# Kernel tuning notes

Measured on AMD Instinct MI355X. Metric: run time of the kernel, lower is better.

The kernel has to match this reference:

```python
import jax, jax.numpy as jnp
import numpy as np

N_LAYERS, D_MODEL, H, D_K, D_V, D_FF, VOCAB = 6, 512, 8, 64, 64, 2048, 32000
B, S = 4, 512
NEG_INF = -jnp.inf


def positional_encoding(seq_len, d_model):
    # Faithful to the (buggy-vs-paper) source: angle = pos / 10000**(2*i/d_model),
    # sin for even i, cos for odd i (i is the raw channel index).
    pos = jnp.arange(seq_len, dtype=jnp.float32)[:, None]
    i = jnp.arange(d_model, dtype=jnp.float32)[None, :]
    angle = pos / jnp.power(10000.0, 2.0 * i / d_model)
    return jnp.where((jnp.arange(d_model) % 2 == 0)[None, :], jnp.sin(angle), jnp.cos(angle))


def layer_norm(x, g, b, eps=1e-5):
    mu = jnp.mean(x, -1, keepdims=True)
    var = jnp.mean((x - mu) ** 2, -1, keepdims=True)
    return (x - mu) * jax.lax.rsqrt(var + eps) * g + b


def mha(q_in, k_in, v_in, wq, wk, wv, wo, q_mask, k_mask, causal):
    # wq/wk: (H, D, D_K), wv: (H, D, D_V), wo: (H*D_V, D)
    q = jnp.einsum('bsd,hdk->bhsk', q_in, wq)
    k = jnp.einsum('btd,hdk->bhtk', k_in, wk)
    v = jnp.einsum('btd,hdk->bhtk', v_in, wv)
    scores = jnp.einsum('bhsk,bhtk->bhst', q, k) / jnp.sqrt(jnp.float32(D_K))
    allowed = q_mask[:, None, :, None] & k_mask[:, None, None, :]  # (B,1,S,T)
    if causal:
        sl, tl = q_in.shape[1], k_in.shape[1]
        allowed = allowed & (jnp.arange(tl)[None, :] <= jnp.arange(sl)[:, None])[None, None]
    scores = jnp.where(allowed, scores, NEG_INF)
    attn = jax.nn.softmax(scores, axis=-1)
    out = jnp.einsum('bhst,bhtk->bshk', attn, v)  # (B,S,H,D_V)
    out = out.reshape(out.shape[0], out.shape[1], H * D_V)
    return out @ wo


def ffn(x, w1, b1, w2, b2):
    return jax.nn.relu(x @ w1 + b1) @ w2 + b2


def setup_inputs() -> dict:
    key = jax.random.key(0)
    ks = iter(jax.random.split(key, 40))
    f = lambda shape, scale: (jax.random.normal(next(ks), shape, dtype=jnp.float32) * scale)
    inp = {
        'src_tokens': jax.random.randint(next(ks), (B, S), 0, VOCAB),
        'tgt_tokens': jax.random.randint(next(ks), (B, S), 0, VOCAB),
        'src_mask': jnp.ones((B, S), dtype=bool),
        'tgt_mask': jnp.ones((B, S), dtype=bool),
        'embed': f((VOCAB, D_MODEL), 0.02),
        'enc_wqkv': f((N_LAYERS, 3, H, D_MODEL, D_K), 0.04),
        'enc_wo': f((N_LAYERS, H * D_V, D_MODEL), 0.04),
        'enc_ff_w1': f((N_LAYERS, D_MODEL, D_FF), 0.02),
        'enc_ff_b1': jnp.zeros((N_LAYERS, D_FF), jnp.float32),
        'enc_ff_w2': f((N_LAYERS, D_FF, D_MODEL), 0.02),
        'enc_ff_b2': jnp.zeros((N_LAYERS, D_MODEL), jnp.float32),
        'enc_ln_g': jnp.ones((N_LAYERS, 2, D_MODEL), jnp.float32),
        'enc_ln_b': jnp.zeros((N_LAYERS, 2, D_MODEL), jnp.float32),
        'dec_wqkv1': f((N_LAYERS, 3, H, D_MODEL, D_K), 0.04),
        'dec_wo1': f((N_LAYERS, H * D_V, D_MODEL), 0.04),
        'dec_wqkv2': f((N_LAYERS, 3, H, D_MODEL, D_K), 0.04),
        'dec_wo2': f((N_LAYERS, H * D_V, D_MODEL), 0.04),
        'dec_ff_w1': f((N_LAYERS, D_MODEL, D_FF), 0.02),
        'dec_ff_b1': jnp.zeros((N_LAYERS, D_FF), jnp.float32),
        'dec_ff_w2': f((N_LAYERS, D_FF, D_MODEL), 0.02),
        'dec_ff_b2': jnp.zeros((N_LAYERS, D_MODEL), jnp.float32),
        'dec_ln_g': jnp.ones((N_LAYERS, 3, D_MODEL), jnp.float32),
        'dec_ln_b': jnp.zeros((N_LAYERS, 3, D_MODEL), jnp.float32),
        'out_w': f((D_MODEL, VOCAB), 0.02),
        'out_b': jnp.zeros((VOCAB,), jnp.float32),
    }
    return inp


def reference(src_tokens, tgt_tokens, src_mask, tgt_mask, embed,
              enc_wqkv, enc_wo, enc_ff_w1, enc_ff_b1, enc_ff_w2, enc_ff_b2, enc_ln_g, enc_ln_b,
              dec_wqkv1, dec_wo1, dec_wqkv2, dec_wo2, dec_ff_w1, dec_ff_b1, dec_ff_w2, dec_ff_b2,
              dec_ln_g, dec_ln_b, out_w, out_b):
    pe = positional_encoding(src_tokens.shape[1], D_MODEL)
    x = embed[src_tokens] + pe[None]
    for i in range(N_LAYERS):
        a = mha(x, x, x, enc_wqkv[i, 0], enc_wqkv[i, 1], enc_wqkv[i, 2], enc_wo[i], src_mask, src_mask, False)
        x = layer_norm(x + a, enc_ln_g[i, 0], enc_ln_b[i, 0])
        x = layer_norm(x + ffn(x, enc_ff_w1[i], enc_ff_b1[i], enc_ff_w2[i], enc_ff_b2[i]), enc_ln_g[i, 1], enc_ln_b[i, 1])
    pe_t = positional_encoding(tgt_tokens.shape[1], D_MODEL)
    y = embed[tgt_tokens] + pe_t[None]
    for i in range(N_LAYERS):
        a = mha(y, y, y, dec_wqkv1[i, 0], dec_wqkv1[i, 1], dec_wqkv1[i, 2], dec_wo1[i], tgt_mask, tgt_mask, True)
        y = layer_norm(y + a, dec_ln_g[i, 0], dec_ln_b[i, 0])
        a = mha(y, x, x, dec_wqkv2[i, 0], dec_wqkv2[i, 1], dec_wqkv2[i, 2], dec_wo2[i], tgt_mask, src_mask, False)
        y = layer_norm(y + a, dec_ln_g[i, 1], dec_ln_b[i, 1])
        y = layer_norm(y + ffn(y, dec_ff_w1[i], dec_ff_b1[i], dec_ff_w2[i], dec_ff_b2[i]), dec_ln_g[i, 2], dec_ln_b[i, 2])
    return y @ out_w + out_b
```

## Files before the change

### kernel.cpp

```cpp
#include <hip/hip_runtime.h>
#include <math.h>


typedef unsigned short u16;
typedef __attribute__((ext_vector_type(8))) short short8;
typedef __attribute__((ext_vector_type(4))) float f32x4;

__device__ __forceinline__ u16 f2bf(float f){
  unsigned u = __float_as_uint(f);
  return (u16)((u + 0x7fffu + ((u >> 16) & 1u)) >> 16);
}

#define GLDS16(gp, lp) __builtin_amdgcn_global_load_lds( \
    (const __attribute__((address_space(1))) unsigned int*)(const void*)(gp), \
    (__attribute__((address_space(3))) unsigned int*)(void*)(lp), 16, 0, 0)

__global__ __launch_bounds__(256) void embed_pe_kernel(
    const int* __restrict__ tok, const float* __restrict__ emb,
    float* __restrict__ out, u16* __restrict__ outh)
{
  int row = blockIdx.x;
  int s = row & 511;
  int t = tok[row];
  #pragma unroll
  for (int j = 0; j < 2; j++){
    int d = threadIdx.x + 256*j;
    float ang = (float)s * powf(10000.0f, -2.0f*(float)d/512.0f);
    float pe = (d & 1) ? cosf(ang) : sinf(ang);
    float v = emb[(size_t)t*512 + d] + pe;
    out[(size_t)row*512 + d] = v;
    outh[(size_t)row*512 + d] = f2bf(v);
  }
}

struct WDesc { const float* W; unsigned long long gs, ds; u16* dst; int K; int nx; int end; };
struct WPack { WDesc d[6]; };

__global__ __launch_bounds__(256) void wcast_multi(WPack P, int nseg){
  int blk = blockIdx.x, s = 0;
  while (s < nseg-1 && blk >= P.d[s].end) s++;
  WDesc D = P.d[s];
  int base = s ? P.d[s-1].end : 0;
  int lb = blk - base;
  int g = lb % D.nx, kt = lb / D.nx;
  __shared__ u16 T[64][65];
  int tid = threadIdx.x;
  const float* Wb = D.W + (size_t)g*D.gs + (size_t)kt*64*D.ds;
  #pragma unroll
  for (int i = 0; i < 16; i++){
    int li = tid + 256*i;
    int kk = li >> 6, c = li & 63;
    T[kk][c] = f2bf(Wb[(size_t)kk*D.ds + c]);
  }
  __syncthreads();
  #pragma unroll
  for (int i = 0; i < 16; i++){
    int lo = tid + 256*i;
    int c = lo >> 6, kk = lo & 63;
    D.dst[(size_t)(g*64 + c)*D.K + kt*64 + kk] = T[kk][c];
  }
}

__global__ __launch_bounds__(256) void flash_attn_kernel(
    const u16* __restrict__ qkv, const u16* __restrict__ vT,
    u16* __restrict__ ctx, int causal)
{
  __shared__ __align__(16) u16 lQ[64*64];
  __shared__ __align__(16) u16 lK[2][64*64];
  __shared__ __align__(16) u16 lV[2][64*64];
  __shared__ __align__(16) u16 lP[4][16*64];
  int tid = threadIdx.x, lane = tid & 63, w = tid >> 6;
  int r16 = lane & 15, l4 = lane >> 4;
  int bh = blockIdx.x >> 3, qb = blockIdx.x & 7;
  int b = bh >> 3, h = bh & 7;
  const u16* qbase = qkv + (size_t)b*512*1536 + h*64;

  #pragma unroll
  for (int i = 0; i < 2; i++){
    int idx = i*256 + tid;
    int r = idx >> 3, c = idx & 7;
    GLDS16(qbase + (size_t)(qb*64 + r)*1536 + ((c ^ (r & 7))*8),
           lQ + (i*256 + w*64)*8);
  }
  auto stageKV = [&](int buf, int tt){
    #pragma unroll
    for (int i = 0; i < 2; i++){
      int idx = i*256 + tid;
      int r = idx >> 3, c = idx & 7;
      GLDS16(qbase + 512 + (size_t)(tt*64 + r)*1536 + ((c ^ (r & 7))*8),
             lK[buf] + (i*256 + w*64)*8);
      GLDS16(vT + ((size_t)bh*64 + r)*512 + tt*64 + ((c ^ (r & 7))*8),
             lV[buf] + (i*256 + w*64)*8);
    }
  };
  stageKV(0, 0);
  __syncthreads();
  short8 qa[2];
  #pragma unroll
  for (int kt = 0; kt < 2; kt++){
    int q = w*16 + r16;
    qa[kt] = *(const short8*)&lQ[q*64 + (((kt*4 + l4) ^ (q & 7))*8)];
  }

  f32x4 o[4];
  float mrow[4], lrow[4];
  #pragma unroll
  for (int j = 0; j < 4; j++){ o[j] = (f32x4){0.f,0.f,0.f,0.f}; mrow[j] = -3e38f; lrow[j] = 0.f; }

  int ntl = causal ? (qb + 1) : 8;
  int buf = 0;
  for (int tt = 0; tt < ntl; tt++){
    if (tt + 1 < ntl) stageKV(buf ^ 1, tt + 1);
    f32x4 s[4];
    #pragma unroll
    for (int ct = 0; ct < 4; ct++) s[ct] = (f32x4){0.f,0.f,0.f,0.f};
    __builtin_amdgcn_s_setprio(1);
    #pragma unroll
    for (int kt = 0; kt < 2; kt++){
      #pragma unroll
      for (int ct = 0; ct < 4; ct++){
        int trow = ct*16 + r16;
        short8 kb = *(const short8*)&lK[buf][trow*64 + (((kt*4 + l4) ^ (trow & 7))*8)];
        s[ct] = __builtin_amdgcn_mfma_f32_16x16x32_bf16(qa[kt], kb, s[ct], 0, 0, 0);
      }
    }
    __builtin_amdgcn_s_setprio(0);
    float p[4][4];
    #pragma unroll
    for (int ct = 0; ct < 4; ct++)
      #pragma unroll
      for (int r = 0; r < 4; r++){
        float v = s[ct][r] * 0.125f;
        if (causal && tt == qb && (ct*16 + r16) > (w*16 + l4*4 + r)) v = -1e30f;
        p[ct][r] = v;
      }
    #pragma unroll
    for (int r = 0; r < 4; r++){
      float pm = fmaxf(fmaxf(p[0][r], p[1][r]), fmaxf(p[2][r], p[3][r]));
      #pragma unroll
      for (int off = 1; off < 16; off <<= 1) pm = fmaxf(pm, __shfl_xor(pm, off));
      float mn = fmaxf(mrow[r], pm);
      float scl = __expf(mrow[r] - mn);
      mrow[r] = mn;
      float rs = 0.f;
      #pragma unroll
      for (int ct = 0; ct < 4; ct++){ p[ct][r] = __expf(p[ct][r] - mn); rs += p[ct][r]; }
      #pragma unroll
      for (int off = 1; off < 16; off <<= 1) rs += __shfl_xor(rs, off);
      lrow[r] = lrow[r]*scl + rs;
      #pragma unroll
      for (int jf = 0; jf < 4; jf++) o[jf][r] *= scl;
    }
    u16* myP = &lP[w][0];
    #pragma unroll
    for (int ct = 0; ct < 4; ct++)
      #pragma unroll
      for (int r = 0; r < 4; r++){
        int q = l4*4 + r, t = ct*16 + r16;
        myP[q*64 + (((t >> 3) ^ (q & 7))*8) + (t & 7)] = f2bf(p[ct][r]);
      }
    __builtin_amdgcn_s_setprio(1);
    #pragma unroll
    for (int kt = 0; kt < 2; kt++){
      short8 pa = *(const short8*)&myP[r16*64 + (((kt*4 + l4) ^ (r16 & 7))*8)];
      #pragma unroll
      for (int jf = 0; jf < 4; jf++){
        int dr = jf*16 + r16;
        short8 vv = *(const short8*)&lV[buf][dr*64 + (((kt*4 + l4) ^ (dr & 7))*8)];
        o[jf] = __builtin_amdgcn_mfma_f32_16x16x32_bf16(pa, vv, o[jf], 0, 0, 0);
      }
    }
    __builtin_amdgcn_s_setprio(0);
    __syncthreads();
    buf ^= 1;
  }
  #pragma unroll
  for (int r = 0; r < 4; r++){
    float inv = 1.0f / lrow[r];
    int q = qb*64 + w*16 + l4*4 + r;
    u16* dst = ctx + (size_t)(b*512 + q)*512 + h*64;
    #pragma unroll
    for (int jf = 0; jf < 4; jf++)
      dst[jf*16 + r16] = f2bf(o[jf][r] * inv);
  }
}

__global__ __launch_bounds__(256) void ln_kernel(
    float* __restrict__ x, const float* __restrict__ res,
    const float* __restrict__ g, const float* __restrict__ bt,
    u16* __restrict__ xh)
{
  int tid = threadIdx.x, lane = tid & 63, wv = tid >> 6;
  int row = blockIdx.x*4 + wv;
  size_t base = (size_t)row*512;
  float v[8]; float sum = 0.f;
  #pragma unroll
  for (int j = 0; j < 8; j++){
    int d = lane + 64*j;
    v[j] = x[base + d] + res[base + d];
    sum += v[j];
  }
  #pragma unroll
  for (int o = 32; o; o >>= 1) sum += __shfl_xor(sum, o);
  float mu = sum * (1.0f/512.0f);
  float vs = 0.f;
  #pragma unroll
  for (int j = 0; j < 8; j++){ float dd = v[j] - mu; vs += dd*dd; }
  #pragma unroll
  for (int o = 32; o; o >>= 1) vs += __shfl_xor(vs, o);
  float rstd = rsqrtf(vs*(1.0f/512.0f) + 1e-5f);
  #pragma unroll
  for (int j = 0; j < 8; j++){
    int d = lane + 64*j;
    float ov = (v[j] - mu)*rstd*g[d] + bt[d];
    x[base + d] = ov;
    xh[base + d] = f2bf(ov);
  }
}

template<int BM, int BN, int WM, int WN, int VOUT>
__global__ __launch_bounds__(WM*WN*64) void mfma_gemm(
    const u16* __restrict__ A, int lda,
    const u16* __restrict__ B, int ldb,
    void* __restrict__ C, int ldc, int cbf,
    const float* __restrict__ bias, int relu, int K, u16* __restrict__ vt)
{
  constexpr int NT  = WM*WN*64;
  constexpr int SM  = BM/WM, SN = BN/WN;
  constexpr int FM  = SM/16, FN = SN/16;
  constexpr int RPS = NT/8;
  constexpr int AG  = BM/RPS, BG = BN/RPS;
  __shared__ __align__(16) u16 lA[2][BM*64];
  __shared__ __align__(16) u16 lB[2][BN*64];
  int tid = threadIdx.x, lane = tid & 63, w = tid >> 6;
  int wm = w / WN, wn = w % WN;
  int r16 = lane & 15, l4 = lane >> 4;
  int sr = (w << 3) + (lane >> 3);
  int sc = lane & 7;
  int scs = sc ^ (sr & 7);
  const u16* Ab = A + (size_t)blockIdx.y*BM*lda + (size_t)sr*lda + scs*8;
  const u16* Bb = B + (size_t)blockIdx.x*BN*ldb + (size_t)sr*ldb + scs*8;
  f32x4 acc[FM][FN];
  #pragma unroll
  for (int i = 0; i < FM; i++)
    #pragma unroll
    for (int j = 0; j < FN; j++)
      acc[i][j] = (f32x4){0.f, 0.f, 0.f, 0.f};

  auto stage = [&](int buf, int kt){
    #pragma unroll
    for (int s = 0; s < AG; s++)
      GLDS16(Ab + (size_t)(s*RPS)*lda + kt, &lA[buf][(s*RPS + (w << 3))*64]);
    #pragma unroll
    for (int s = 0; s < BG; s++)
      GLDS16(Bb + (size_t)(s*RPS)*ldb + kt, &lB[buf][(s*RPS + (w << 3))*64]);
  };
  stage(0, 0);
  int nk = K >> 6, cur = 0;
  for (int kt = 0; kt < nk; kt++){
    __syncthreads();
    if (kt + 1 < nk) stage(cur ^ 1, (kt + 1) << 6);
    #pragma unroll
    for (int ks = 0; ks < 2; ks++){
      short8 av[FM], bv[FN];
      #pragma unroll
      for (int i = 0; i < FM; i++){
        int row = wm*SM + i*16 + r16;
        av[i] = *(const short8*)&lA[cur][row*64 + (((ks*4 + l4) ^ (row & 7))*8)];
      }
      #pragma unroll
      for (int j = 0; j < FN; j++){
        int row = wn*SN + j*16 + r16;
        bv[j] = *(const short8*)&lB[cur][row*64 + (((ks*4 + l4) ^ (row & 7))*8)];
      }
      #pragma unroll
      for (int i = 0; i < FM; i++)
        #pragma unroll
        for (int j = 0; j < FN; j++)
          acc[i][j] = __builtin_amdgcn_mfma_f32_16x16x32_bf16(av[i], bv[j], acc[i][j], 0, 0, 0);
    }
    cur ^= 1;
  }

  if constexpr (VOUT){
    int nblk = blockIdx.x * BN;
    if (nblk >= 1024){
      constexpr int TP = BM + 4;
      u16* T = (u16*)&lA[0][0];
      __syncthreads();
      #pragma unroll
      for (int i = 0; i < FM; i++){
        int t0 = wm*SM + i*16 + l4*4;
        #pragma unroll
        for (int j = 0; j < FN; j++){
          int d = wn*SN + j*16 + r16;
          unsigned q01 = (unsigned)f2bf(acc[i][j][0]) | ((unsigned)f2bf(acc[i][j][1]) << 16);
          unsigned q23 = (unsigned)f2bf(acc[i][j][2]) | ((unsigned)f2bf(acc[i][j][3]) << 16);
          uint2 pk; pk.x = q01; pk.y = q23;
          *(uint2*)&T[d*TP + t0] = pk;
        }
      }
      __syncthreads();
      int h = (nblk - 1024) >> 6;
      int b = (blockIdx.y * BM) >> 9;
      int t0g = (blockIdx.y * BM) & 511;
      u16* dst = vt + (size_t)(b*8 + h)*64*512;
      constexpr int TQL = (BM == 128) ? 5 : 4;
      constexpr int NIT = (BM*64) / (NT*4);
      #pragma unroll
      for (int it = 0; it < NIT; it++){
        int idx = it*NT + tid;
        int d = idx >> TQL, tq = (idx & ((1 << TQL) - 1))*4;
        *(uint2*)&dst[(size_t)d*512 + t0g + tq] = *(const uint2*)&T[d*TP + tq];
      }
      return;
    }
  }

  int m0 = blockIdx.y*BM + wm*SM, n0 = blockIdx.x*BN + wn*SN;
  int r4 = l4*4;
  #pragma unroll
  for (int i = 0; i < FM; i++){
    #pragma unroll
    for (int j = 0; j < FN; j++){
      int col = n0 + j*16 + r16;
      float bi = bias ? bias[col] : 0.f;
      #pragma unroll
      for (int r = 0; r < 4; r++){
        int rowg = m0 + i*16 + r4 + r;
        float o = acc[i][j][r] + bi;
        if (relu) o = fmaxf(o, 0.f);
        if (cbf) ((u16*)C)[(size_t)rowg*ldc + col] = f2bf(o);
        else     ((float*)C)[(size_t)rowg*ldc + col] = o;
      }
    }
  }
}

__global__ __launch_bounds__(256) void xattn_qkv_gemm(
    const u16* __restrict__ Ay, const u16* __restrict__ Ax,
    const u16* __restrict__ Bt, u16* __restrict__ C, u16* __restrict__ vt)
{
  constexpr int BM=64, BN=64, WM=2, WN=2, NT=256;
  constexpr int SM=BM/WM, SN=BN/WN, FM=SM/16, FN=SN/16, RPS=NT/8;
  constexpr int AG=BM/RPS, BG=BN/RPS;
  __shared__ __align__(16) u16 lA[2][BM*64];
  __shared__ __align__(16) u16 lB[2][BN*64];
  int tid = threadIdx.x, lane = tid & 63, w = tid >> 6;
  int wm = w / WN, wn = w % WN;
  int r16 = lane & 15, l4 = lane >> 4;
  int sr = (w << 3) + (lane >> 3);
  int sc = lane & 7;
  int scs = sc ^ (sr & 7);
  int z = blockIdx.z;
  const u16* A = (z == 0) ? Ay : Ax;
  const u16* Ab = A + (size_t)blockIdx.y*BM*512 + (size_t)sr*512 + scs*8;
  const u16* Bb = Bt + (size_t)(z*512 + blockIdx.x*BN)*512 + (size_t)sr*512 + scs*8;
  f32x4 acc[FM][FN];
  #pragma unroll
  for (int i = 0; i < FM; i++)
    #pragma unroll
    for (int j = 0; j < FN; j++)
      acc[i][j] = (f32x4){0.f, 0.f, 0.f, 0.f};
  auto stage = [&](int buf, int kt){
    #pragma unroll
    for (int s = 0; s < AG; s++)
      GLDS16(Ab + (size_t)(s*RPS)*512 + kt, &lA[buf][(s*RPS + (w << 3))*64]);
    #pragma unroll
    for (int s = 0; s < BG; s++)
      GLDS16(Bb + (size_t)(s*RPS)*512 + kt, &lB[buf][(s*RPS + (w << 3))*64]);
  };
  stage(0, 0);
  int cur = 0;
  for (int kt = 0; kt < 8; kt++){
    __syncthreads();
    if (kt + 1 < 8) stage(cur ^ 1, (kt + 1) << 6);
    #pragma unroll
    for (int ks = 0; ks < 2; ks++){
      short8 av[FM], bv[FN];
      #pragma unroll
      for (int i = 0; i < FM; i++){
        int row = wm*SM + i*16 + r16;
        av[i] = *(const short8*)&lA[cur][row*64 + (((ks*4 + l4) ^ (row & 7))*8)];
      }
      #pragma unroll
      for (int j = 0; j < FN; j++){
        int row = wn*SN + j*16 + r16;
        bv[j] = *(const short8*)&lB[cur][row*64 + (((ks*4 + l4) ^ (row & 7))*8)];
      }
      #pragma unroll
      for (int i = 0; i < FM; i++)
        #pragma unroll
        for (int j = 0; j < FN; j++)
          acc[i][j] = __builtin_amdgcn_mfma_f32_16x16x32_bf16(av[i], bv[j], acc[i][j], 0, 0, 0);
    }
    cur ^= 1;
  }
  if (z == 2){
    constexpr int TP = BM + 4;
    u16* T = (u16*)&lA[0][0];
    __syncthreads();
    #pragma unroll
    for (int i = 0; i < FM; i++){
      int t0 = wm*SM + i*16 + l4*4;
      #pragma unroll
      for (int j = 0; j < FN; j++){
        int d = wn*SN + j*16 + r16;
        unsigned q01 = (unsigned)f2bf(acc[i][j][0]) | ((unsigned)f2bf(acc[i][j][1]) << 16);
        unsigned q23 = (unsigned)f2bf(acc[i][j][2]) | ((unsigned)f2bf(acc[i][j][3]) << 16);
        uint2 pk; pk.x = q01; pk.y = q23;
        *(uint2*)&T[d*TP + t0] = pk;
      }
    }
    __syncthreads();
    int h = blockIdx.x;
    int b = (blockIdx.y * BM) >> 9;
    int t0g = (blockIdx.y * BM) & 511;
    u16* dst = vt + (size_t)(b*8 + h)*64*512;
    #pragma unroll
    for (int it = 0; it < 1; it++){ }
    #pragma unroll
    for (int it = 0; it < (BM*64)/(NT*4); it++){
      int idx = it*NT + tid;
      int d = idx >> 4, tq = (idx & 15)*4;
      *(uint2*)&dst[(size_t)d*512 + t0g + tq] = *(const uint2*)&T[d*TP + tq];
    }
    return;
  }
  int m0 = blockIdx.y*BM + wm*SM, n0 = z*512 + blockIdx.x*BN + wn*SN;
  int r4 = l4*4;
  #pragma unroll
  for (int i = 0; i < FM; i++)
    #pragma unroll
    for (int j = 0; j < FN; j++)
      #pragma unroll
      for (int r = 0; r < 4; r++){
        int rowg = m0 + i*16 + r4 + r;
        C[(size_t)rowg*1536 + n0 + j*16 + r16] = f2bf(acc[i][j][r]);
      }
}

extern "C" void kernel_launch(void* const* d_in, const int* in_sizes, int n_in,
                              void* d_out, int out_size, void* d_ws, size_t ws_size,
                              hipStream_t stream)
{
  (void)in_sizes; (void)n_in; (void)out_size; (void)ws_size;
  const int*   src_tok   = (const int*)  d_in[0];
  const int*   tgt_tok   = (const int*)  d_in[1];
  const float* emb       = (const float*)d_in[4];
  const float* enc_wqkv  = (const float*)d_in[5];
  const float* enc_wo    = (const float*)d_in[6];
  const float* enc_ff_w1 = (const float*)d_in[7];
  const float* enc_ff_b1 = (const float*)d_in[8];
  const float* enc_ff_w2 = (const float*)d_in[9];
  const float* enc_ff_b2 = (const float*)d_in[10];
  const float* enc_ln_g  = (const float*)d_in[11];
  const float* enc_ln_b  = (const float*)d_in[12];
  const float* dec_wqkv1 = (const float*)d_in[13];
  const float* dec_wo1   = (const float*)d_in[14];
  const float* dec_wqkv2 = (const float*)d_in[15];
  const float* dec_wo2   = (const float*)d_in[16];
  const float* dec_ff_w1 = (const float*)d_in[17];
  const float* dec_ff_b1 = (const float*)d_in[18];
  const float* dec_ff_w2 = (const float*)d_in[19];
  const float* dec_ff_b2 = (const float*)d_in[20];
  const float* dec_ln_g  = (const float*)d_in[21];
  const float* dec_ln_b  = (const float*)d_in[22];
  const float* out_w     = (const float*)d_in[23];
  const float* out_b     = (const float*)d_in[24];
  float* outp = (float*)d_out;

  const size_t MB = 1024*1024;
  char* wsb = (char*)d_ws;
  float* xb     = (float*)(wsb + 0*MB);
  float* yb     = (float*)(wsb + 4*MB);
  u16*   xh     = (u16*)  (wsb + 8*MB);
  u16*   ctxb   = (u16*)  (wsb + 10*MB);
  u16*   yh     = (u16*)  (wsb + 12*MB);
  u16*   qkvb   = (u16*)  (wsb + 14*MB);
  u16*   vT     = (u16*)  (wsb + 20*MB);
  u16*   hid    = (u16*)  (wsb + 14*MB);
  u16*   sQKV   = (u16*)  (wsb + 22*MB);
  u16*   sWO    = (u16*)  (wsb + 23*MB + 512*1024);
  u16*   sFF1   = (u16*)  (wsb + 24*MB);
  u16*   sFF2   = (u16*)  (wsb + 26*MB);
  float* proj   = (float*)(wsb + 28*MB);
  u16*   wvbuf  = (u16*)  (wsb + 0*MB);

  auto g64 = [&](const u16* A,int lda,const u16* B,int ldb,void* C,int ldc,
                 int cbf,const float* bias,int relu,int M,int N,int K){
    mfma_gemm<64,64,2,2,0><<<dim3(N/64, M/64), 256, 0, stream>>>(
        A,lda,B,ldb,C,ldc,cbf,bias,relu,K,nullptr);
  };
  auto gqkv = [&](const u16* A,const u16* B,u16* C,u16* vt,int M){
    mfma_gemm<128,64,2,2,1><<<dim3(24, M/128), 256, 0, stream>>>(
        A,512,B,512,C,1536,1,nullptr,0,512,vt);
  };
  auto g12864 = [&](const u16* A,int lda,const u16* B,int ldb,void* C,int ldc,
                    int cbf,const float* bias,int relu,int M,int N,int K){
    mfma_gemm<128,64,2,2,0><<<dim3(N/64, M/128), 256, 0, stream>>>(
        A,lda,B,ldb,C,ldc,cbf,bias,relu,K,nullptr);
  };
  auto g128 = [&](const u16* A,int lda,const u16* B,int ldb,void* C,int ldc,
                  int cbf,const float* bias,int relu,int M,int N,int K){
    mfma_gemm<128,128,2,2,0><<<dim3(N/128, M/128), 256, 0, stream>>>(
        A,lda,B,ldb,C,ldc,cbf,bias,relu,K,nullptr);
  };
  auto ln = [&](float* x, const float* g, const float* b, u16* oh){
    ln_kernel<<<512, 256, 0, stream>>>(x, proj, g, b, oh);
  };
  auto cast = [&](WDesc* segs, int n){
    WPack P; int tot = 0;
    for (int s = 0; s < n; s++){
      tot += segs[s].nx * (segs[s].K/64);
      segs[s].end = tot;
      P.d[s] = segs[s];
    }
    for (int s = n; s < 6; s++) P.d[s] = P.d[0];
    wcast_multi<<<tot, 256, 0, stream>>>(P, n);
  };

  const size_t WQKV_L = (size_t)3*8*512*64;

  embed_pe_kernel<<<2048, 256, 0, stream>>>(src_tok, emb, xb, xh);
  for (int i = 0; i < 6; i++){
    WDesc segs[4] = {
      {enc_wqkv + i*WQKV_L,            32768, 64,   sQKV, 512,  24, 0},
      {enc_wo   + (size_t)i*262144,    64,    512,  sWO,  512,  8,  0},
      {enc_ff_w1+ (size_t)i*512*2048,  64,    2048, sFF1, 512,  32, 0},
      {enc_ff_w2+ (size_t)i*2048*512,  64,    512,  sFF2, 2048, 8,  0}};
    cast(segs, 4);
    gqkv(xh, sQKV, qkvb, vT, 2048);
    flash_attn_kernel<<<256, 256, 0, stream>>>(qkvb, vT, ctxb, 0);
    g64(ctxb, 512, sWO, 512, proj, 512, 0, nullptr, 0, 2048, 512, 512);
    ln(xb, enc_ln_g + i*1024,       enc_ln_b + i*1024,       xh);
    g12864(xh, 512, sFF1, 512, hid, 2048, 1, enc_ff_b1 + i*2048, 1, 2048, 2048, 512);
    g64(hid, 2048, sFF2, 2048, proj, 512, 0, enc_ff_b2 + i*512, 0, 2048, 512, 2048);
    ln(xb, enc_ln_g + i*1024 + 512, enc_ln_b + i*1024 + 512, xh);
  }

  embed_pe_kernel<<<2048, 256, 0, stream>>>(tgt_tok, emb, yb, yh);
  for (int i = 0; i < 6; i++){
    WDesc segs1[4] = {
      {dec_wqkv1 + i*WQKV_L,           32768, 64,   sQKV, 512,  24, 0},
      {dec_wo1   + (size_t)i*262144,   64,    512,  sWO,  512,  8,  0},
      {dec_ff_w1 + (size_t)i*512*2048, 64,    2048, sFF1, 512,  32, 0},
      {dec_ff_w2 + (size_t)i*2048*512, 64,    512,  sFF2, 2048, 8,  0}};
    cast(segs1, 4);
    gqkv(yh, sQKV, qkvb, vT, 2048);
    flash_attn_kernel<<<256, 256, 0, stream>>>(qkvb, vT, ctxb, 1);
    g64(ctxb, 512, sWO, 512, proj, 512, 0, nullptr, 0, 2048, 512, 512);
    ln(yb, dec_ln_g + i*1536,        dec_ln_b + i*1536,        yh);
    WDesc segs2[2] = {
      {dec_wqkv2 + i*WQKV_L,         32768, 64,  sQKV, 512, 24, 0},
      {dec_wo2   + (size_t)i*262144, 64,    512, sWO,  512, 8,  0}};
    cast(segs2, 2);
    xattn_qkv_gemm<<<dim3(8, 32, 3), 256, 0, stream>>>(yh, xh, sQKV, qkvb, vT);
    flash_attn_kernel<<<256, 256, 0, stream>>>(qkvb, vT, ctxb, 0);
    g64(ctxb, 512, sWO, 512, proj, 512, 0, nullptr, 0, 2048, 512, 512);
    ln(yb, dec_ln_g + i*1536 + 512,  dec_ln_b + i*1536 + 512,  yh);
    g12864(yh, 512, sFF1, 512, hid, 2048, 1, dec_ff_b1 + i*2048, 1, 2048, 2048, 512);
    g64(hid, 2048, sFF2, 2048, proj, 512, 0, dec_ff_b2 + i*512, 0, 2048, 512, 2048);
    ln(yb, dec_ln_g + i*1536 + 1024, dec_ln_b + i*1536 + 1024, yh);
  }

  const int c0s[5] = {0, 8192, 16384, 24576, 32000};
  for (int c = 0; c < 4; c++){
    int c0 = c0s[c], NC = c0s[c+1] - c0;
    WDesc seg[1] = {{out_w + c0, 64, 32000, wvbuf, 512, NC/64, 0}};
    cast(seg, 1);
    g128(yh, 512, wvbuf, 512, outp + c0, 32000, 0, out_b + c0, 0, 2048, NC, 512);
  }
}
```

Before: 1.526 ms.

## Fuse fp32 weight cast into GEMM B-operand staging, drop separate cast kernels

Removes the separate wcast_multi kernel that converted fp32 weights to transposed bf16 buffers before each layer's GEMMs. The GEMM kernels now read fp32 weights directly into registers, convert them to bf16 and write them swizzled into LDS, with register prefetch overlapping the MFMA loop. The output projection becomes a single 128x64-tile GEMM instead of four chunked cast+GEMM pairs. This saves launches and one global round trip of the weights. The cost is strided fp32 loads in every GEMM block, repeated across M-blocks instead of done once, which may hurt GEMMs with many row tiles such as the vocab projection.

```diff
diff --git a/kernel.cpp b/kernel.cpp
--- a/kernel.cpp
+++ b/kernel.cpp
@@ -30,34 +30,6 @@
     float v = emb[(size_t)t*512 + d] + pe;
     out[(size_t)row*512 + d] = v;
     outh[(size_t)row*512 + d] = f2bf(v);
-  }
-}
-
-struct WDesc { const float* W; unsigned long long gs, ds; u16* dst; int K; int nx; int end; };
-struct WPack { WDesc d[6]; };
-
-__global__ __launch_bounds__(256) void wcast_multi(WPack P, int nseg){
-  int blk = blockIdx.x, s = 0;
-  while (s < nseg-1 && blk >= P.d[s].end) s++;
-  WDesc D = P.d[s];
-  int base = s ? P.d[s-1].end : 0;
-  int lb = blk - base;
-  int g = lb % D.nx, kt = lb / D.nx;
-  __shared__ u16 T[64][65];
-  int tid = threadIdx.x;
-  const float* Wb = D.W + (size_t)g*D.gs + (size_t)kt*64*D.ds;
-  #pragma unroll
-  for (int i = 0; i < 16; i++){
-    int li = tid + 256*i;
-    int kk = li >> 6, c = li & 63;
-    T[kk][c] = f2bf(Wb[(size_t)kk*D.ds + c]);
-  }
-  __syncthreads();
-  #pragma unroll
-  for (int i = 0; i < 16; i++){
-    int lo = tid + 256*i;
-    int c = lo >> 6, kk = lo & 63;
-    D.dst[(size_t)(g*64 + c)*D.K + kt*64 + kk] = T[kk][c];
   }
 }
 
@@ -218,18 +190,20 @@
   }
 }
 
-template<int BM, int BN, int WM, int WN, int VOUT>
+template<int BM, int WM, int WN, int VOUT>
 __global__ __launch_bounds__(WM*WN*64) void mfma_gemm(
     const u16* __restrict__ A, int lda,
-    const u16* __restrict__ B, int ldb,
+    const float* __restrict__ W, size_t gs, size_t ds,
     void* __restrict__ C, int ldc, int cbf,
     const float* __restrict__ bias, int relu, int K, u16* __restrict__ vt)
 {
+  constexpr int BN  = 64;
   constexpr int NT  = WM*WN*64;
+  static_assert(NT == 256, "B-staging assumes 4 waves");
   constexpr int SM  = BM/WM, SN = BN/WN;
   constexpr int FM  = SM/16, FN = SN/16;
   constexpr int RPS = NT/8;
-  constexpr int AG  = BM/RPS, BG = BN/RPS;
+  constexpr int AG  = BM/RPS;
   __shared__ __align__(16) u16 lA[2][BM*64];
   __shared__ __align__(16) u16 lB[2][BN*64];
   int tid = threadIdx.x, lane = tid & 63, w = tid >> 6;
@@ -239,7 +213,30 @@
   int sc = lane & 7;
   int scs = sc ^ (sr & 7);
   const u16* Ab = A + (size_t)blockIdx.y*BM*lda + (size_t)sr*lda + scs*8;
-  const u16* Bb = B + (size_t)blockIdx.x*BN*ldb + (size_t)sr*ldb + scs*8;
+  int bn  = tid & 63;
+  int bk0 = (tid >> 6) * 16;
+  int n0  = blockIdx.x * 64;
+  const float* Wp = W + (size_t)((n0 + bn) >> 6)*gs + (bn & 63);
+  float fB[16];
+  auto loadB = [&](int kt){
+    #pragma unroll
+    for (int j = 0; j < 16; j++) fB[j] = Wp[(size_t)(kt + bk0 + j)*ds];
+  };
+  auto writeB = [&](int buf){
+    unsigned d[8];
+    #pragma unroll
+    for (int j = 0; j < 8; j++)
+      d[j] = (unsigned)f2bf(fB[2*j]) | ((unsigned)f2bf(fB[2*j+1]) << 16);
+    int c0 = bk0 >> 3;
+    *(uint4*)&lB[buf][bn*64 + (( c0    ^ (bn & 7)) << 3)] = make_uint4(d[0],d[1],d[2],d[3]);
+    *(uint4*)&lB[buf][bn*64 + (((c0+1) ^ (bn & 7)) << 3)] = make_uint4(d[4],d[5],d[6],d[7]);
+  };
+  auto stageA = [&](int buf, int kt){
+    #pragma unroll
+    for (int s = 0; s < AG; s++)
+      GLDS16(Ab + (size_t)(s*RPS)*lda + kt, &lA[buf][(s*RPS + (w << 3))*64]);
+  };
+
   f32x4 acc[FM][FN];
   #pragma unroll
   for (int i = 0; i < FM; i++)
@@ -247,19 +244,11 @@
     for (int j = 0; j < FN; j++)
       acc[i][j] = (f32x4){0.f, 0.f, 0.f, 0.f};
 
-  auto stage = [&](int buf, int kt){
-    #pragma unroll
-    for (int s = 0; s < AG; s++)
-      GLDS16(Ab + (size_t)(s*RPS)*lda + kt, &lA[buf][(s*RPS + (w << 3))*64]);
-    #pragma unroll
-    for (int s = 0; s < BG; s++)
-      GLDS16(Bb + (size_t)(s*RPS)*ldb + kt, &lB[buf][(s*RPS + (w << 3))*64]);
-  };
-  stage(0, 0);
+  loadB(0); writeB(0); stageA(0, 0);
   int nk = K >> 6, cur = 0;
   for (int kt = 0; kt < nk; kt++){
     __syncthreads();
-    if (kt + 1 < nk) stage(cur ^ 1, (kt + 1) << 6);
+    if (kt + 1 < nk){ loadB((kt + 1) << 6); stageA(cur ^ 1, (kt + 1) << 6); }
     #pragma unroll
     for (int ks = 0; ks < 2; ks++){
       short8 av[FM], bv[FN];
@@ -279,6 +268,7 @@
         for (int j = 0; j < FN; j++)
           acc[i][j] = __builtin_amdgcn_mfma_f32_16x16x32_bf16(av[i], bv[j], acc[i][j], 0, 0, 0);
     }
+    if (kt + 1 < nk) writeB(cur ^ 1);
     cur ^= 1;
   }
 
@@ -317,13 +307,13 @@
     }
   }
 
-  int m0 = blockIdx.y*BM + wm*SM, n0 = blockIdx.x*BN + wn*SN;
+  int m0 = blockIdx.y*BM + wm*SM, n0o = blockIdx.x*BN + wn*SN;
   int r4 = l4*4;
   #pragma unroll
   for (int i = 0; i < FM; i++){
     #pragma unroll
     for (int j = 0; j < FN; j++){
-      int col = n0 + j*16 + r16;
+      int col = n0o + j*16 + r16;
       float bi = bias ? bias[col] : 0.f;
       #pragma unroll
       for (int r = 0; r < 4; r++){
@@ -339,11 +329,11 @@
 
 __global__ __launch_bounds__(256) void xattn_qkv_gemm(
     const u16* __restrict__ Ay, const u16* __restrict__ Ax,
-    const u16* __restrict__ Bt, u16* __restrict__ C, u16* __restrict__ vt)
+    const float* __restrict__ Wq, u16* __restrict__ C, u16* __restrict__ vt)
 {
   constexpr int BM=64, BN=64, WM=2, WN=2, NT=256;
   constexpr int SM=BM/WM, SN=BN/WN, FM=SM/16, FN=SN/16, RPS=NT/8;
-  constexpr int AG=BM/RPS, BG=BN/RPS;
+  constexpr int AG=BM/RPS;
   __shared__ __align__(16) u16 lA[2][BM*64];
   __shared__ __align__(16) u16 lB[2][BN*64];
   int tid = threadIdx.x, lane = tid & 63, w = tid >> 6;
@@ -355,26 +345,40 @@
   int z = blockIdx.z;
   const u16* A = (z == 0) ? Ay : Ax;
   const u16* Ab = A + (size_t)blockIdx.y*BM*512 + (size_t)sr*512 + scs*8;
-  const u16* Bb = Bt + (size_t)(z*512 + blockIdx.x*BN)*512 + (size_t)sr*512 + scs*8;
+  int bn  = tid & 63;
+  int bk0 = (tid >> 6) * 16;
+  int n0  = blockIdx.x * 64;
+  const float* Wp = Wq + (size_t)z*262144 + (size_t)((n0 + bn) >> 6)*32768 + (bn & 63);
+  float fB[16];
+  auto loadB = [&](int kt){
+    #pragma unroll
+    for (int j = 0; j < 16; j++) fB[j] = Wp[(size_t)(kt + bk0 + j)*64];
+  };
+  auto writeB = [&](int buf){
+    unsigned d[8];
+    #pragma unroll
+    for (int j = 0; j < 8; j++)
+      d[j] = (unsigned)f2bf(fB[2*j]) | ((unsigned)f2bf(fB[2*j+1]) << 16);
+    int c0 = bk0 >> 3;
+    *(uint4*)&lB[buf][bn*64 + (( c0    ^ (bn & 7)) << 3)] = make_uint4(d[0],d[1],d[2],d[3]);
+    *(uint4*)&lB[buf][bn*64 + (((c0+1) ^ (bn & 7)) << 3)] = make_uint4(d[4],d[5],d[6],d[7]);
+  };
+  auto stageA = [&](int buf, int kt){
+    #pragma unroll
+    for (int s = 0; s < AG; s++)
+      GLDS16(Ab + (size_t)(s*RPS)*512 + kt, &lA[buf][(s*RPS + (w << 3))*64]);
+  };
   f32x4 acc[FM][FN];
   #pragma unroll
   for (int i = 0; i < FM; i++)
     #pragma unroll
     for (int j = 0; j < FN; j++)
       acc[i][j] = (f32x4){0.f, 0.f, 0.f, 0.f};
-  auto stage = [&](int buf, int kt){
-    #pragma unroll
-    for (int s = 0; s < AG; s++)
-      GLDS16(Ab + (size_t)(s*RPS)*512 + kt, &lA[buf][(s*RPS + (w << 3))*64]);
-    #pragma unroll
-    for (int s = 0; s < BG; s++)
-      GLDS16(Bb + (size_t)(s*RPS)*512 + kt, &lB[buf][(s*RPS + (w << 3))*64]);
-  };
-  stage(0, 0);
+  loadB(0); writeB(0); stageA(0, 0);
   int cur = 0;
   for (int kt = 0; kt < 8; kt++){
     __syncthreads();
-    if (kt + 1 < 8) stage(cur ^ 1, (kt + 1) << 6);
+    if (kt + 1 < 8){ loadB((kt + 1) << 6); stageA(cur ^ 1, (kt + 1) << 6); }
     #pragma unroll
     for (int ks = 0; ks < 2; ks++){
       short8 av[FM], bv[FN];
@@ -394,6 +398,7 @@
         for (int j = 0; j < FN; j++)
           acc[i][j] = __builtin_amdgcn_mfma_f32_16x16x32_bf16(av[i], bv[j], acc[i][j], 0, 0, 0);
     }
+    if (kt + 1 < 8) writeB(cur ^ 1);
     cur ^= 1;
   }
   if (z == 2){
@@ -418,8 +423,6 @@
     int t0g = (blockIdx.y * BM) & 511;
     u16* dst = vt + (size_t)(b*8 + h)*64*512;
     #pragma unroll
-    for (int it = 0; it < 1; it++){ }
-    #pragma unroll
     for (int it = 0; it < (BM*64)/(NT*4); it++){
       int idx = it*NT + tid;
       int d = idx >> 4, tq = (idx & 15)*4;
@@ -427,7 +430,7 @@
     }
     return;
   }
-  int m0 = blockIdx.y*BM + wm*SM, n0 = z*512 + blockIdx.x*BN + wn*SN;
+  int m0 = blockIdx.y*BM + wm*SM, n0o = z*512 + blockIdx.x*BN + wn*SN;
   int r4 = l4*4;
   #pragma unroll
   for (int i = 0; i < FM; i++)
@@ -436,7 +439,7 @@
       #pragma unroll
       for (int r = 0; r < 4; r++){
         int rowg = m0 + i*16 + r4 + r;
-        C[(size_t)rowg*1536 + n0 + j*16 + r16] = f2bf(acc[i][j][r]);
+        C[(size_t)rowg*1536 + n0o + j*16 + r16] = f2bf(acc[i][j][r]);
       }
 }
 
@@ -480,95 +483,63 @@
   u16*   qkvb   = (u16*)  (wsb + 14*MB);
   u16*   vT     = (u16*)  (wsb + 20*MB);
   u16*   hid    = (u16*)  (wsb + 14*MB);
-  u16*   sQKV   = (u16*)  (wsb + 22*MB);
-  u16*   sWO    = (u16*)  (wsb + 23*MB + 512*1024);
-  u16*   sFF1   = (u16*)  (wsb + 24*MB);
-  u16*   sFF2   = (u16*)  (wsb + 26*MB);
   float* proj   = (float*)(wsb + 28*MB);
-  u16*   wvbuf  = (u16*)  (wsb + 0*MB);
-
-  auto g64 = [&](const u16* A,int lda,const u16* B,int ldb,void* C,int ldc,
-                 int cbf,const float* bias,int relu,int M,int N,int K){
-    mfma_gemm<64,64,2,2,0><<<dim3(N/64, M/64), 256, 0, stream>>>(
-        A,lda,B,ldb,C,ldc,cbf,bias,relu,K,nullptr);
-  };
-  auto gqkv = [&](const u16* A,const u16* B,u16* C,u16* vt,int M){
-    mfma_gemm<128,64,2,2,1><<<dim3(24, M/128), 256, 0, stream>>>(
-        A,512,B,512,C,1536,1,nullptr,0,512,vt);
-  };
-  auto g12864 = [&](const u16* A,int lda,const u16* B,int ldb,void* C,int ldc,
-                    int cbf,const float* bias,int relu,int M,int N,int K){
-    mfma_gemm<128,64,2,2,0><<<dim3(N/64, M/128), 256, 0, stream>>>(
-        A,lda,B,ldb,C,ldc,cbf,bias,relu,K,nullptr);
-  };
-  auto g128 = [&](const u16* A,int lda,const u16* B,int ldb,void* C,int ldc,
-                  int cbf,const float* bias,int relu,int M,int N,int K){
-    mfma_gemm<128,128,2,2,0><<<dim3(N/128, M/128), 256, 0, stream>>>(
-        A,lda,B,ldb,C,ldc,cbf,bias,relu,K,nullptr);
+
+  auto g64 = [&](const u16* A,int lda,const float* W,size_t gs,size_t ds,
+                 void* C,int ldc,int cbf,const float* bias,int relu,
+                 int M,int N,int K){
+    mfma_gemm<64,2,2,0><<<dim3(N/64, M/64), 256, 0, stream>>>(
+        A,lda,W,gs,ds,C,ldc,cbf,bias,relu,K,nullptr);
+  };
+  auto g128 = [&](const u16* A,int lda,const float* W,size_t gs,size_t ds,
+                  void* C,int ldc,int cbf,const float* bias,int relu,
+                  int M,int N,int K){
+    mfma_gemm<128,2,2,0><<<dim3(N/64, M/128), 256, 0, stream>>>(
+        A,lda,W,gs,ds,C,ldc,cbf,bias,relu,K,nullptr);
+  };
+  auto gqkv = [&](const u16* A,const float* W,u16* C,u16* vt){
+    mfma_gemm<128,2,2,1><<<dim3(24, 16), 256, 0, stream>>>(
+        A,512,W,32768,64,C,1536,1,nullptr,0,512,vt);
   };
   auto ln = [&](float* x, const float* g, const float* b, u16* oh){
     ln_kernel<<<512, 256, 0, stream>>>(x, proj, g, b, oh);
   };
-  auto cast = [&](WDesc* segs, int n){
-    WPack P; int tot = 0;
-    for (int s = 0; s < n; s++){
-      tot += segs[s].nx * (segs[s].K/64);
-      segs[s].end = tot;
-      P.d[s] = segs[s];
-    }
-    for (int s = n; s < 6; s++) P.d[s] = P.d[0];
-    wcast_multi<<<tot, 256, 0, stream>>>(P, n);
-  };
 
   const size_t WQKV_L = (size_t)3*8*512*64;
 
   embed_pe_kernel<<<2048, 256, 0, stream>>>(src_tok, emb, xb, xh);
   for (int i = 0; i < 6; i++){
-    WDesc segs[4] = {
-      {enc_wqkv + i*WQKV_L,            32768, 64,   sQKV, 512,  24, 0},
-      {enc_wo   + (size_t)i*262144,    64,    512,  sWO,  512,  8,  0},
-      {enc_ff_w1+ (size_t)i*512*2048,  64,    2048, sFF1, 512,  32, 0},
-      {enc_ff_w2+ (size_t)i*2048*512,  64,    512,  sFF2, 2048, 8,  0}};
-    cast(segs, 4);
-    gqkv(xh, sQKV, qkvb, vT, 2048);
+    gqkv(xh, enc_wqkv + i*WQKV_L, qkvb, vT);
     flash_attn_kernel<<<256, 256, 0, stream>>>(qkvb, vT, ctxb, 0);
-    g64(ctxb, 512, sWO, 512, proj, 512, 0, nullptr, 0, 2048, 512, 512);
+    g64(ctxb, 512, enc_wo + (size_t)i*262144, 64, 512, proj, 512, 0,
+        nullptr, 0, 2048, 512, 512);
     ln(xb, enc_ln_g + i*1024,       enc_ln_b + i*1024,       xh);
-    g12864(xh, 512, sFF1, 512, hid, 2048, 1, enc_ff_b1 + i*2048, 1, 2048, 2048, 512);
-    g64(hid, 2048, sFF2, 2048, proj, 512, 0, enc_ff_b2 + i*512, 0, 2048, 512, 2048);
+    g128(xh, 512, enc_ff_w1 + (size_t)i*512*2048, 64, 2048, hid, 2048, 1,
+         enc_ff_b1 + i*2048, 1, 2048, 2048, 512);
+    g64(hid, 2048, enc_ff_w2 + (size_t)i*2048*512, 64, 512, proj, 512, 0,
+        enc_ff_b2 + i*512, 0, 2048, 512, 2048);
     ln(xb, enc_ln_g + i*1024 + 512, enc_ln_b + i*1024 + 512, xh);
   }
 
   embed_pe_kernel<<<2048, 256, 0, stream>>>(tgt_tok, emb, yb, yh);
   for (int i = 0; i < 6; i++){
-    WDesc segs1[4] = {
-      {dec_wqkv1 + i*WQKV_L,           32768, 64,   sQKV, 512,  24, 0},
-      {dec_wo1   + (size_t)i*262144,   64,    512,  sWO,  512,  8,  0},
-      {dec_ff_w1 + (size_t)i*512*2048, 64,    2048, sFF1, 512,  32, 0},
-      {dec_ff_w2 + (size_t)i*2048*512, 64,    512,  sFF2, 2048, 8,  0}};
-    cast(segs1, 4);
-    gqkv(yh, sQKV, qkvb, vT, 2048);
+    gqkv(yh, dec_wqkv1 + i*WQKV_L, qkvb, vT);
     flash_attn_kernel<<<256, 256, 0, stream>>>(qkvb, vT, ctxb, 1);
-    g64(ctxb, 512, sWO, 512, proj, 512, 0, nullptr, 0, 2048, 512, 512);
+    g64(ctxb, 512, dec_wo1 + (size_t)i*262144, 64, 512, proj, 512, 0,
+        nullptr, 0, 2048, 512, 512);
     ln(yb, dec_ln_g + i*1536,        dec_ln_b + i*1536,        yh);
-    WDesc segs2[2] = {
-      {dec_wqkv2 + i*WQKV_L,         32768, 64,  sQKV, 512, 24, 0},
-      {dec_wo2   + (size_t)i*262144, 64,    512, sWO,  512, 8,  0}};
-    cast(segs2, 2);
-    xattn_qkv_gemm<<<dim3(8, 32, 3), 256, 0, stream>>>(yh, xh, sQKV, qkvb, vT);
+    xattn_qkv_gemm<<<dim3(8, 32, 3), 256, 0, stream>>>(
+        yh, xh, dec_wqkv2 + i*WQKV_L, qkvb, vT);
     flash_attn_kernel<<<256, 256, 0, stream>>>(qkvb, vT, ctxb, 0);
-    g64(ctxb, 512, sWO, 512, proj, 512, 0, nullptr, 0, 2048, 512, 512);
+    g64(ctxb, 512, dec_wo2 + (size_t)i*262144, 64, 512, proj, 512, 0,
+        nullptr, 0, 2048, 512, 512);
     ln(yb, dec_ln_g + i*1536 + 512,  dec_ln_b + i*1536 + 512,  yh);
-    g12864(yh, 512, sFF1, 512, hid, 2048, 1, dec_ff_b1 + i*2048, 1, 2048, 2048, 512);
-    g64(hid, 2048, sFF2, 2048, proj, 512, 0, dec_ff_b2 + i*512, 0, 2048, 512, 2048);
+    g128(yh, 512, dec_ff_w1 + (size_t)i*512*2048, 64, 2048, hid, 2048, 1,
+         dec_ff_b1 + i*2048, 1, 2048, 2048, 512);
+    g64(hid, 2048, dec_ff_w2 + (size_t)i*2048*512, 64, 512, proj, 512, 0,
+        dec_ff_b2 + i*512, 0, 2048, 512, 2048);
     ln(yb, dec_ln_g + i*1536 + 1024, dec_ln_b + i*1536 + 1024, yh);
   }
 
-  const int c0s[5] = {0, 8192, 16384, 24576, 32000};
-  for (int c = 0; c < 4; c++){
-    int c0 = c0s[c], NC = c0s[c+1] - c0;
-    WDesc seg[1] = {{out_w + c0, 64, 32000, wvbuf, 512, NC/64, 0}};
-    cast(seg, 1);
-    g128(yh, 512, wvbuf, 512, outp + c0, 32000, 0, out_b + c0, 0, 2048, NC, 512);
-  }
-}
+  g128(yh, 512, out_w, 64, 32000, outp, 32000, 0, out_b, 0, 2048, 32000, 512);
+}
```

New measurement: 1.947 ms. +27.6%, slower.
